# Kernel optimization log

Hardware: AMD Instinct MI355X
Metric: run time of the kernel (lower is better)

The kernel has to match this reference:

```python
import jax, jax.numpy as jnp
import numpy as np

NV = 8192   # number of nodes
NE = 8192   # number of edges
IN_V = 512
OUT_V = 512
IN_E = 512
A_COEF = 0.5  # self.a ; self.b = 1 - a


def setup_inputs() -> dict:
    key = jax.random.key(0)
    k = jax.random.split(key, 8)
    stdv = 1.0 / np.sqrt(OUT_V)
    return {
        "H_v": jax.random.normal(k[0], (NV, IN_V), dtype=jnp.float32),
        "H_e": jax.random.normal(k[1], (NE, IN_E), dtype=jnp.float32),
        "adj_e": jax.random.uniform(k[2], (NE, NE), dtype=jnp.float32),
        "adj_v": jax.random.uniform(k[3], (NV, NV), dtype=jnp.float32),
        "T": jax.random.uniform(k[4], (NV, NE), dtype=jnp.float32),
        "weight": jax.random.uniform(k[5], (IN_V, OUT_V), minval=-stdv, maxval=stdv, dtype=jnp.float32),
        "p": jax.random.normal(k[6], (1, IN_E), dtype=jnp.float32),
        "bias": jax.random.uniform(k[7], (OUT_V,), minval=-stdv, maxval=stdv, dtype=jnp.float32),
    }


def reference(H_v, H_e, adj_e, adj_v, T, weight, p, bias):
    # node_layer=True path of GraphConvolution.forward
    # gate: per-edge scalar from H_e @ p^T  -> [Ne]
    gate = (H_e @ p.T)[:, 0]
    # T @ diag(gate) @ T^T computed as broadcast column-scale (same math,
    # avoids materializing the Ne x Ne diagonal)
    multiplier1 = (T * gate[None, :]) @ T.T            # [Nv, Nv]
    eye = jnp.eye(multiplier1.shape[0], dtype=multiplier1.dtype)
    M1 = eye + (1.0 - eye) * multiplier1
    adjusted_A = M1 * adj_v
    H_v_weight = H_v @ weight                          # [Nv, out_v]
    output = adjusted_A @ H_v_weight
    output1 = adj_v @ H_v_weight
    output = output * A_COEF + output1 * (1.0 - A_COEF)
    ret = output + bias
    return (ret, H_e)
```

## Files before the change

kernel.cpp:

```cpp
#include <hip/hip_runtime.h>
#include <hip/hip_bf16.h>

typedef __attribute__((ext_vector_type(4))) float  f32x4;
typedef __attribute__((ext_vector_type(8))) short  s16x8;
typedef __attribute__((ext_vector_type(4))) short  s16x4;

#define NV 8192
#define NE 8192
#define DIM 512

__device__ inline short f2bf(float x) {
    unsigned u = __float_as_uint(x);
    u += 0x7fffu + ((u >> 16) & 1u);
    return (short)(u >> 16);
}
__device__ inline float bf2f(short s) {
    return __uint_as_float(((unsigned)(unsigned short)s) << 16);
}

__global__ void gate_kernel(const float* __restrict__ He, const float* __restrict__ p,
                            float* __restrict__ gate) {
    int row  = blockIdx.x * 4 + (threadIdx.x >> 6);
    int lane = threadIdx.x & 63;
    const float* r = He + (size_t)row * DIM + lane * 8;
    float4 a0 = *(const float4*)r;
    float4 a1 = *(const float4*)(r + 4);
    float4 p0 = *(const float4*)(p + lane * 8);
    float4 p1 = *(const float4*)(p + lane * 8 + 4);
    float s = a0.x*p0.x + a0.y*p0.y + a0.z*p0.z + a0.w*p0.w
            + a1.x*p1.x + a1.y*p1.y + a1.z*p1.z + a1.w*p1.w;
    #pragma unroll
    for (int off = 32; off; off >>= 1) s += __shfl_down(s, off);
    if (lane == 0) gate[row] = s;
}

__global__ void convert_T(const float* __restrict__ T, const float* __restrict__ gate,
                          short* __restrict__ Tg, short* __restrict__ Tb) {
    size_t gid  = (size_t)blockIdx.x * blockDim.x + threadIdx.x;
    size_t base = gid * 8;
    int col = (int)(base & (NE - 1));
    float4 t0 = *(const float4*)(T + base);
    float4 t1 = *(const float4*)(T + base + 4);
    float4 g0 = *(const float4*)(gate + col);
    float4 g1 = *(const float4*)(gate + col + 4);
    s16x8 vb, vg;
    vb[0]=f2bf(t0.x); vb[1]=f2bf(t0.y); vb[2]=f2bf(t0.z); vb[3]=f2bf(t0.w);
    vb[4]=f2bf(t1.x); vb[5]=f2bf(t1.y); vb[6]=f2bf(t1.z); vb[7]=f2bf(t1.w);
    vg[0]=f2bf(t0.x*g0.x); vg[1]=f2bf(t0.y*g0.y); vg[2]=f2bf(t0.z*g0.z); vg[3]=f2bf(t0.w*g0.w);
    vg[4]=f2bf(t1.x*g1.x); vg[5]=f2bf(t1.y*g1.y); vg[6]=f2bf(t1.z*g1.z); vg[7]=f2bf(t1.w*g1.w);
    *(s16x8*)(Tb + base) = vb;
    *(s16x8*)(Tg + base) = vg;
}

__global__ void to_bf16(const float* __restrict__ in, short* __restrict__ out) {
    size_t base = ((size_t)blockIdx.x * blockDim.x + threadIdx.x) * 8;
    float4 a = *(const float4*)(in + base);
    float4 b = *(const float4*)(in + base + 4);
    s16x8 v;
    v[0]=f2bf(a.x); v[1]=f2bf(a.y); v[2]=f2bf(a.z); v[3]=f2bf(a.w);
    v[4]=f2bf(b.x); v[5]=f2bf(b.y); v[6]=f2bf(b.z); v[7]=f2bf(b.w);
    *(s16x8*)(out + base) = v;
}

__global__ void wT_bf16(const float* __restrict__ W, short* __restrict__ WT) {
    __shared__ short t[64][65];
    int rb = blockIdx.x, cb = blockIdx.y;
    int c = threadIdx.x & 63, r0 = threadIdx.x >> 6;
    #pragma unroll
    for (int i = 0; i < 16; ++i) {
        int r = i * 4 + r0;
        t[r][c] = f2bf(W[(size_t)(rb * 64 + r) * DIM + cb * 64 + c]);
    }
    __syncthreads();
    #pragma unroll
    for (int i = 0; i < 16; ++i) {
        int r = i * 4 + r0;
        WT[(size_t)(cb * 64 + r) * DIM + rb * 64 + c] = t[c][r];
    }
}

template<int EPI>
__global__ __launch_bounds__(256)
void gemm_bt(const short* __restrict__ A, const short* __restrict__ B,
             int M, int N, int K,
             short* __restrict__ Cb,
             const float* __restrict__ bias, float* __restrict__ Cf) {
    __shared__ short As[128 * 32];
    __shared__ short Bs[128 * 32];

    int nwg = gridDim.x;
    int bid = blockIdx.x;
    int cpx = nwg >> 3;
    bid = (bid & 7) * cpx + (bid >> 3);

    const int nbn = N >> 7;
    const int bm = (bid / nbn) << 7;
    const int bn = (bid % nbn) << 7;
    const int tid  = threadIdx.x;
    const int lane = tid & 63;
    const int wave = tid >> 6;
    const int wrow = (wave >> 1) * 64;
    const int wcol = (wave & 1) * 64;

    f32x4 acc[4][4] = {};

    const int lrow = lane >> 2;
    const int lcol = ((lane & 3) ^ ((lrow >> 1) & 3)) * 8;

    for (int k0 = 0; k0 < K; k0 += 32) {
        #pragma unroll
        for (int it = 0; it < 2; ++it) {
            int chunk = it * 4 + wave;
            int row = chunk * 16 + lrow;
            __builtin_amdgcn_global_load_lds(
                (const __attribute__((address_space(1))) void*)(A + (size_t)(bm + row) * K + k0 + lcol),
                (__attribute__((address_space(3))) void*)(As + chunk * 512), 16, 0, 0);
            __builtin_amdgcn_global_load_lds(
                (const __attribute__((address_space(1))) void*)(B + (size_t)(bn + row) * K + k0 + lcol),
                (__attribute__((address_space(3))) void*)(Bs + chunk * 512), 16, 0, 0);
        }
        __syncthreads();

        const int fr = lane & 15;
        const int sw = (fr >> 1) & 3;
        const int sa = ((lane >> 4) ^ sw) * 8;
        s16x8 af[4], bfr[4];
        #pragma unroll
        for (int i = 0; i < 4; ++i) {
            af[i]  = *(const s16x8*)&As[(wrow + i * 16 + fr) * 32 + sa];
            bfr[i] = *(const s16x8*)&Bs[(wcol + i * 16 + fr) * 32 + sa];
        }
        #pragma unroll
        for (int i = 0; i < 4; ++i)
            #pragma unroll
            for (int j = 0; j < 4; ++j)
                acc[i][j] = __builtin_amdgcn_mfma_f32_16x16x32_bf16(af[i], bfr[j], acc[i][j], 0, 0, 0);
        __syncthreads();
    }

    const int fr = lane & 15, fq = (lane >> 4) * 4;
    #pragma unroll
    for (int i = 0; i < 4; ++i) {
        #pragma unroll
        for (int j = 0; j < 4; ++j) {
            int col = bn + wcol + j * 16 + fr;
            #pragma unroll
            for (int v = 0; v < 4; ++v) {
                int row = bm + wrow + i * 16 + fq + v;
                float d = acc[i][j][v];
                if (EPI == 1) Cf[(size_t)row * N + col] = d + bias[col];
                else          Cb[(size_t)row * N + col] = f2bf(d);
            }
        }
    }
}

#define FENCE asm volatile("" ::: "memory")
#define BAR   do { FENCE; __builtin_amdgcn_s_barrier(); FENCE; } while (0)
#define MFMA16(I0, J0)                                                                       \
    _Pragma("unroll") for (int x = 0; x < 4; ++x)                                            \
    _Pragma("unroll") for (int y = 0; y < 2; ++y)                                            \
    _Pragma("unroll") for (int s = 0; s < 2; ++s)                                            \
        acc[(I0)+x][(J0)+y] = __builtin_amdgcn_mfma_f32_16x16x32_bf16(                       \
            af[x][s], bf[(J0)+y][s], acc[(I0)+x][(J0)+y], 0, 0, 0);

#define GEMM256_CORE(NIT, KMASK)                                                             \
    stageA(0, 0, 0); stageA(0, 1, 0);                                                        \
    stageB(0, 0, 0); stageB(0, 1, 0);                                                        \
    stageB(1, 0, 1); stageB(1, 1, 1);                                                        \
    asm volatile("s_waitcnt vmcnt(4)" ::: "memory");                                         \
    __builtin_amdgcn_s_barrier();                                                            \
    FENCE;                                                                                   \
    _Pragma("unroll 1")                                                                      \
    for (int it = 0; it < (NIT); ++it) {                                                     \
        const int kt = it * 2;                                                               \
        _Pragma("unroll") for (int x = 0; x < 4; ++x) { af[x][0] = lda(A0o, x, 0); af[x][1] = lda(A0o, x, 1); } \
        _Pragma("unroll") for (int y = 0; y < 2; ++y) { bf[y][0] = ldb(B0o, y, 0); bf[y][1] = ldb(B0o, y, 1); } \
        stageA(1, 0, kt + 1);                                                                \
        asm volatile("s_waitcnt lgkmcnt(8)" ::: "memory");                                   \
        BAR; __builtin_amdgcn_s_setprio(1); MFMA16(0, 0) __builtin_amdgcn_s_setprio(0); BAR; \
        _Pragma("unroll") for (int y = 0; y < 2; ++y) { bf[2+y][0] = ldb(B0o, 2+y, 0); bf[2+y][1] = ldb(B0o, 2+y, 1); } \
        stageA(1, 1, kt + 1);                                                                \
        BAR; __builtin_amdgcn_s_setprio(1); MFMA16(0, 2) __builtin_amdgcn_s_setprio(0); BAR; \
        _Pragma("unroll") for (int x = 0; x < 4; ++x) { af[x][0] = lda(A0o, 4+x, 0); af[x][1] = lda(A0o, 4+x, 1); } \
        stageB(0, 0, kt + 2);                                                                \
        BAR; __builtin_amdgcn_s_setprio(1); MFMA16(4, 0) __builtin_amdgcn_s_setprio(0); BAR; \
        stageB(0, 1, kt + 2);                                                                \
        BAR; __builtin_amdgcn_s_setprio(1); MFMA16(4, 2) __builtin_amdgcn_s_setprio(0);      \
        asm volatile("s_waitcnt vmcnt(4)" ::: "memory"); BAR;                                \
        _Pragma("unroll") for (int x = 0; x < 4; ++x) { af[x][0] = lda(A1o, x, 0); af[x][1] = lda(A1o, x, 1); } \
        _Pragma("unroll") for (int y = 0; y < 2; ++y) { bf[y][0] = ldb(B1o, y, 0); bf[y][1] = ldb(B1o, y, 1); } \
        stageA(0, 0, kt + 2);                                                                \
        asm volatile("s_waitcnt lgkmcnt(8)" ::: "memory");                                   \
        BAR; __builtin_amdgcn_s_setprio(1); MFMA16(0, 0) __builtin_amdgcn_s_setprio(0); BAR; \
        _Pragma("unroll") for (int y = 0; y < 2; ++y) { bf[2+y][0] = ldb(B1o, 2+y, 0); bf[2+y][1] = ldb(B1o, 2+y, 1); } \
        stageA(0, 1, kt + 2);                                                                \
        BAR; __builtin_amdgcn_s_setprio(1); MFMA16(0, 2) __builtin_amdgcn_s_setprio(0); BAR; \
        _Pragma("unroll") for (int x = 0; x < 4; ++x) { af[x][0] = lda(A1o, 4+x, 0); af[x][1] = lda(A1o, 4+x, 1); } \
        stageB(1, 0, kt + 3);                                                                \
        BAR; __builtin_amdgcn_s_setprio(1); MFMA16(4, 0) __builtin_amdgcn_s_setprio(0); BAR; \
        stageB(1, 1, kt + 3);                                                                \
        BAR; __builtin_amdgcn_s_setprio(1); MFMA16(4, 2) __builtin_amdgcn_s_setprio(0);      \
        asm volatile("s_waitcnt vmcnt(4)" ::: "memory"); BAR;                                \
    }                                                                                        \
    asm volatile("s_waitcnt vmcnt(0)" ::: "memory");                                         \
    BAR;

#define GEMM256_PRELUDE(KMASK)                                                               \
    const int tid  = threadIdx.x;                                                            \
    const int wave = tid >> 6;                                                               \
    const int lane = tid & 63;                                                               \
    const int wm = wave >> 2;                                                                \
    const int wn = wave & 3;                                                                 \
    const int fr = lane & 15;                                                                \
    const int kq = lane >> 4;                                                                \
    const int lr = lane >> 3;                                                                \
    const int lsl = (lane & 7) ^ lr;                                                         \
    const int A0o = wm * 8192;                                                               \
    const int A1o = 16384 + wm * 8192;                                                       \
    const int B0o = 32768 + ((wn >> 1) << 13);                                               \
    const int B1o = B0o + 16384;                                                             \
    const short* aSrc = A + (size_t)(bm + wave * 8 + lr) * 8192 + kb + lsl * 8;              \
    const short* bSrc = B + (size_t)(bn + wave * 8 + lr) * 8192 + kb + lsl * 8;              \
    auto stageA = [&](int buf, int h, int kt) {                                              \
        const short* s0 = aSrc + ((size_t)h << 20) + ((kt << 6) & (KMASK));                  \
        short* d = &lds[buf * 16384 + h * 8192 + wave * 512];                                \
        __builtin_amdgcn_global_load_lds((const __attribute__((address_space(1))) void*)s0,  \
            (__attribute__((address_space(3))) void*)d, 16, 0, 0);                           \
        __builtin_amdgcn_global_load_lds((const __attribute__((address_space(1))) void*)(s0 + (size_t)(64 * 8192)), \
            (__attribute__((address_space(3))) void*)(d + 4096), 16, 0, 0);                  \
    };                                                                                       \
    auto stageB = [&](int buf, int h, int kt) {                                              \
        const short* s0 = bSrc + ((size_t)h << 20) + ((kt << 6) & (KMASK));                  \
        short* d = &lds[32768 + buf * 16384 + h * 8192 + wave * 512];                        \
        __builtin_amdgcn_global_load_lds((const __attribute__((address_space(1))) void*)s0,  \
            (__attribute__((address_space(3))) void*)d, 16, 0, 0);                           \
        __builtin_amdgcn_global_load_lds((const __attribute__((address_space(1))) void*)(s0 + (size_t)(64 * 8192)), \
            (__attribute__((address_space(3))) void*)(d + 4096), 16, 0, 0);                  \
    };                                                                                       \
    auto lda = [&](int base, int i, int ks) -> s16x8 {                                       \
        int rl = i * 16 + fr;                                                                \
        int slot = ((ks << 2) + kq) ^ (rl & 7);                                              \
        return *(const s16x8*)&lds[base + rl * 64 + slot * 8];                               \
    };                                                                                       \
    auto ldb = [&](int base, int j, int ks) -> s16x8 {                                       \
        int rl = ((wn & 1) << 6) + j * 16 + fr;                                              \
        int slot = ((ks << 2) + kq) ^ (rl & 7);                                              \
        return *(const s16x8*)&lds[base + rl * 64 + slot * 8];                               \
    };                                                                                       \
    f32x4 acc[8][4] = {};                                                                    \
    s16x8 af[4][2], bf[4][2];

__global__ __launch_bounds__(512, 2)
void gemm256(const short* __restrict__ A, const short* __restrict__ B,
             const float* __restrict__ adj, short* __restrict__ Cb) {
    __shared__ short lds[65536];

    int b = blockIdx.x;
    b = (b & 7) * 64 + (b >> 3);
    int bi, bj;
    if (b < 496) {
        int rem = b;
        bi = 0;
        while (rem >= 31 - bi) { rem -= 31 - bi; ++bi; }
        bj = bi + 1 + rem;
    } else {
        bi = bj = b - 496;
    }
    const int bm = bi << 8;
    const int bn = bj << 8;
    const int kb = 0;

    GEMM256_PRELUDE(8191)
    GEMM256_CORE(64, 8191)

    const int fq = kq << 2;
    #pragma unroll
    for (int i = 0; i < 8; ++i) {
        int rl0 = wm * 128 + i * 16 + fq;
        #pragma unroll
        for (int j = 0; j < 4; ++j) {
            int cl = wn * 64 + j * 16 + fr;
            #pragma unroll
            for (int v = 0; v < 4; ++v) {
                int rl = rl0 + v;
                lds[rl * 256 + (cl ^ ((rl & 7) << 3))] = f2bf(acc[i][j][v]);
            }
        }
    }
    BAR;

    const int rloc = tid >> 5;
    const int cc   = (tid & 31) * 8;
    #pragma unroll 4
    for (int m = 0; m < 16; ++m) {
        int r = m * 16 + rloc;
        s16x8 mv = *(const s16x8*)&lds[r * 256 + (cc ^ ((r & 7) << 3))];
        const float* arow = adj + (size_t)(bm + r) * 8192 + bn + cc;
        float4 a0 = *(const float4*)arow;
        float4 a1 = *(const float4*)(arow + 4);
        float av[8] = {a0.x,a0.y,a0.z,a0.w,a1.x,a1.y,a1.z,a1.w};
        s16x8 o;
        #pragma unroll
        for (int e = 0; e < 8; ++e) {
            float cv = av[e] * (0.5f * bf2f(mv[e]) + 0.5f);
            if (bm == bn && r == cc + e) cv = av[e];
            o[e] = f2bf(cv);
        }
        *(s16x8*)&Cb[(size_t)(bm + r) * 8192 + bn + cc] = o;
    }

    if (bm != bn) {
        #pragma unroll 1
        for (int h = 0; h < 2; ++h) {
            BAR;
            if ((wn >> 1) == h) {
                #pragma unroll
                for (int i = 0; i < 8; ++i) {
                    int r0 = wm * 128 + i * 16 + fq;
                    #pragma unroll
                    for (int j = 0; j < 4; ++j) {
                        int c = ((wn & 1) << 6) + j * 16 + fr;
                        s16x4 o4;
                        o4[0] = f2bf(acc[i][j][0]); o4[1] = f2bf(acc[i][j][1]);
                        o4[2] = f2bf(acc[i][j][2]); o4[3] = f2bf(acc[i][j][3]);
                        *(s16x4*)&lds[c * 264 + r0] = o4;
                    }
                }
            }
            BAR;
            const int r0 = (tid & 31) * 8;
            #pragma unroll 2
            for (int itr = 0; itr < 8; ++itr) {
                int c = itr * 16 + (tid >> 5);
                s16x8 mv = *(const s16x8*)&lds[c * 264 + r0];
                const float* arow = adj + (size_t)(bn + h * 128 + c) * 8192 + bm + r0;
                float4 a0 = *(const float4*)arow;
                float4 a1 = *(const float4*)(arow + 4);
                float av[8] = {a0.x,a0.y,a0.z,a0.w,a1.x,a1.y,a1.z,a1.w};
                s16x8 o;
                #pragma unroll
                for (int e = 0; e < 8; ++e)
                    o[e] = f2bf(av[e] * (0.5f * bf2f(mv[e]) + 0.5f));
                *(s16x8*)&Cb[(size_t)(bn + h * 128 + c) * 8192 + bm + r0] = o;
            }
        }
    }
}

__global__ __launch_bounds__(512, 2)
void gemm256_ks(const short* __restrict__ A, const short* __restrict__ B,
                float* __restrict__ part) {
    __shared__ short lds[65536];

    int b = blockIdx.x;
    const int t  = b >> 4;
    const int ks = b & 15;
    const int bm = (16 + t) << 8;
    const int bn = bm;
    const int kb = ks << 9;

    GEMM256_PRELUDE(511)
    GEMM256_CORE(4, 511)

    float* po = part + (size_t)(t * 16 + ks) * 65536;
    const int fq = kq << 2;
    #pragma unroll
    for (int i = 0; i < 8; ++i) {
        #pragma unroll
        for (int j = 0; j < 4; ++j) {
            int C = wn * 64 + j * 16 + fr;
            #pragma unroll
            for (int v = 0; v < 4; ++v) {
                int R = wm * 128 + i * 16 + fq + v;
                po[R * 256 + C] = acc[i][j][v];
            }
        }
    }
}

__global__ void reduce_diag(const float* __restrict__ part, const float* __restrict__ adj,
                            short* __restrict__ Cb) {
    int b = blockIdx.x;
    int t = b >> 5, sub = b & 31;
    int base = sub * 2048 + threadIdx.x * 8;
    int r = base >> 8, c = base & 255;
    const float* ps = part + (size_t)t * 16 * 65536 + base;
    float s[8] = {};
    #pragma unroll
    for (int ks = 0; ks < 16; ++ks) {
        f32x4 a = *(const f32x4*)(ps + (size_t)ks * 65536);
        f32x4 bq = *(const f32x4*)(ps + (size_t)ks * 65536 + 4);
        s[0]+=a[0]; s[1]+=a[1]; s[2]+=a[2]; s[3]+=a[3];
        s[4]+=bq[0]; s[5]+=bq[1]; s[6]+=bq[2]; s[7]+=bq[3];
    }
    int gr = (16 + t) * 256 + r, gc0 = (16 + t) * 256 + c;
    const float* arow = adj + (size_t)gr * 8192 + gc0;
    float4 a0 = *(const float4*)arow, a1 = *(const float4*)(arow + 4);
    float av[8] = {a0.x,a0.y,a0.z,a0.w,a1.x,a1.y,a1.z,a1.w};
    s16x8 o;
    #pragma unroll
    for (int e = 0; e < 8; ++e) {
        float cv = av[e] * (0.5f * s[e] + 0.5f);
        if (gr == gc0 + e) cv = av[e];
        o[e] = f2bf(cv);
    }
    *(s16x8*)&Cb[(size_t)gr * 8192 + gc0] = o;
}

__global__ __launch_bounds__(512, 2)
void gemm_fin(const short* __restrict__ A, const short* __restrict__ B,
              float* __restrict__ part) {
    __shared__ short lds[65536];

    int b = blockIdx.x;
    const int ks  = b & 3;
    const int bmi = (b >> 2) & 31;
    const int bni = b >> 7;
    const int bm = bmi << 8;
    const int bn = bni << 8;
    const int kb = ks << 11;

    GEMM256_PRELUDE(2047)
    GEMM256_CORE(16, 2047)

    float* po = part + ((size_t)(bmi * 2 + bni) * 4 + ks) * 65536;
    const int fq = kq << 2;
    #pragma unroll
    for (int i = 0; i < 8; ++i) {
        #pragma unroll
        for (int j = 0; j < 4; ++j) {
            int C = wn * 64 + j * 16 + fr;
            #pragma unroll
            for (int v = 0; v < 4; ++v) {
                int R = wm * 128 + i * 16 + fq + v;
                po[R * 256 + C] = acc[i][j][v];
            }
        }
    }
}

__global__ void reduce_out(const float* __restrict__ part, const float* __restrict__ bias,
                           float* __restrict__ out) {
    size_t g = ((size_t)blockIdx.x * 256 + threadIdx.x) * 8;
    int r = (int)(g >> 9);
    int c = (int)(g & 511);
    int tile = ((r >> 8) << 1) + (c >> 8);
    size_t inner = (size_t)(r & 255) * 256 + (c & 255);
    const float* ps = part + ((size_t)tile * 4) * 65536 + inner;
    float s[8] = {};
    #pragma unroll
    for (int ks = 0; ks < 4; ++ks) {
        f32x4 a = *(const f32x4*)(ps + (size_t)ks * 65536);
        f32x4 bq = *(const f32x4*)(ps + (size_t)ks * 65536 + 4);
        s[0]+=a[0]; s[1]+=a[1]; s[2]+=a[2]; s[3]+=a[3];
        s[4]+=bq[0]; s[5]+=bq[1]; s[6]+=bq[2]; s[7]+=bq[3];
    }
    float4 b0 = *(const float4*)(bias + c);
    float4 b1 = *(const float4*)(bias + c + 4);
    float bv[8] = {b0.x,b0.y,b0.z,b0.w,b1.x,b1.y,b1.z,b1.w};
    f32x4 o0, o1;
    o0[0]=s[0]+bv[0]; o0[1]=s[1]+bv[1]; o0[2]=s[2]+bv[2]; o0[3]=s[3]+bv[3];
    o1[0]=s[4]+bv[4]; o1[1]=s[5]+bv[5]; o1[2]=s[6]+bv[6]; o1[3]=s[7]+bv[7];
    *(f32x4*)(out + g) = o0;
    *(f32x4*)(out + g + 4) = o1;
}

extern "C" void kernel_launch(void* const* d_in, const int* in_sizes, int n_in,
                              void* d_out, int out_size, void* d_ws, size_t ws_size,
                              hipStream_t stream) {
    const float* Hv   = (const float*)d_in[0];
    const float* He   = (const float*)d_in[1];
    const float* adjv = (const float*)d_in[3];
    const float* T    = (const float*)d_in[4];
    const float* Wf   = (const float*)d_in[5];
    const float* p    = (const float*)d_in[6];
    const float* bias = (const float*)d_in[7];
    float* out = (float*)d_out;

    char* ws = (char*)d_ws;
    float* gate = (float*)(ws);
    short* Hvb  = (short*)(ws + 32768);
    short* Wt   = (short*)(ws + 8421376);
    short* Tg   = (short*)(ws + 16809984);
    short* Tb   = (short*)(ws + 151027712);
    short* Cb   = (short*)(ws + 285245440);
    short* WTb  = (short*)(ws + 285245440);
    float* part = (float*)(ws + 16809984);
    float* part2 = (float*)(ws + 16809984);

    hipMemcpyAsync(out + (size_t)NV * DIM, He, (size_t)NE * DIM * sizeof(float),
                   hipMemcpyDeviceToDevice, stream);

    gate_kernel<<<NE / 4, 256, 0, stream>>>(He, p, gate);
    convert_T<<<(NV * (NE / 8)) / 256, 256, 0, stream>>>(T, gate, Tg, Tb);
    to_bf16<<<(NV * DIM / 8) / 256, 256, 0, stream>>>(Hv, Hvb);
    wT_bf16<<<dim3(8, 8), 256, 0, stream>>>(Wf, WTb);

    gemm_bt<2><<<(DIM / 128) * (NV / 128), 256, 0, stream>>>(
        WTb, Hvb, DIM, NV, DIM, Wt, nullptr, nullptr);

    gemm256<<<512, 512, 0, stream>>>(Tg, Tb, adjv, Cb);
    gemm256_ks<<<256, 512, 0, stream>>>(Tg, Tb, part);
    reduce_diag<<<512, 256, 0, stream>>>(part, adjv, Cb);

    gemm_fin<<<256, 512, 0, stream>>>(Cb, Wt, part2);
    reduce_out<<<(NV * DIM / 8) / 256, 256, 0, stream>>>(part2, bias, out);
}
```

Baseline: 725.9 us.

## Triple-buffer A tiles in LDS with rotating slots for deeper prefetch

The A operand moves from a double-buffered to a triple-buffered LDS ring with three rotating slot bases (cA, cB, cC). Each A tile is now staged two k-steps ahead instead of one, and the vmcnt waits are relaxed from 4 to 8 so more global-to-LDS loads can stay in flight. B stays double-buffered and is moved to a higher LDS offset. LDS per block grows from 128KB to 160KB, which uses the full CU LDS and rules out a second resident block.

```diff
diff --git a/kernel.cpp b/kernel.cpp
--- a/kernel.cpp
+++ b/kernel.cpp
@@ -165,43 +165,46 @@
             af[x][s], bf[(J0)+y][s], acc[(I0)+x][(J0)+y], 0, 0, 0);
 
 #define GEMM256_CORE(NIT, KMASK)                                                             \
+    int cA = 0, cB = 16384, cC = 32768;                                                      \
     stageA(0, 0, 0); stageA(0, 1, 0);                                                        \
     stageB(0, 0, 0); stageB(0, 1, 0);                                                        \
+    stageA(16384, 0, 1); stageA(16384, 1, 1);                                                \
     stageB(1, 0, 1); stageB(1, 1, 1);                                                        \
-    asm volatile("s_waitcnt vmcnt(4)" ::: "memory");                                         \
+    asm volatile("s_waitcnt vmcnt(8)" ::: "memory");                                         \
     __builtin_amdgcn_s_barrier();                                                            \
     FENCE;                                                                                   \
     _Pragma("unroll 1")                                                                      \
     for (int it = 0; it < (NIT); ++it) {                                                     \
         const int kt = it * 2;                                                               \
-        _Pragma("unroll") for (int x = 0; x < 4; ++x) { af[x][0] = lda(A0o, x, 0); af[x][1] = lda(A0o, x, 1); } \
+        _Pragma("unroll") for (int x = 0; x < 4; ++x) { af[x][0] = lda(cA, x, 0); af[x][1] = lda(cA, x, 1); } \
         _Pragma("unroll") for (int y = 0; y < 2; ++y) { bf[y][0] = ldb(B0o, y, 0); bf[y][1] = ldb(B0o, y, 1); } \
-        stageA(1, 0, kt + 1);                                                                \
+        stageA(cC, 0, kt + 2);                                                               \
         asm volatile("s_waitcnt lgkmcnt(8)" ::: "memory");                                   \
         BAR; __builtin_amdgcn_s_setprio(1); MFMA16(0, 0) __builtin_amdgcn_s_setprio(0); BAR; \
         _Pragma("unroll") for (int y = 0; y < 2; ++y) { bf[2+y][0] = ldb(B0o, 2+y, 0); bf[2+y][1] = ldb(B0o, 2+y, 1); } \
-        stageA(1, 1, kt + 1);                                                                \
+        stageA(cC, 1, kt + 2);                                                               \
         BAR; __builtin_amdgcn_s_setprio(1); MFMA16(0, 2) __builtin_amdgcn_s_setprio(0); BAR; \
-        _Pragma("unroll") for (int x = 0; x < 4; ++x) { af[x][0] = lda(A0o, 4+x, 0); af[x][1] = lda(A0o, 4+x, 1); } \
+        _Pragma("unroll") for (int x = 0; x < 4; ++x) { af[x][0] = lda(cA, 4+x, 0); af[x][1] = lda(cA, 4+x, 1); } \
         stageB(0, 0, kt + 2);                                                                \
         BAR; __builtin_amdgcn_s_setprio(1); MFMA16(4, 0) __builtin_amdgcn_s_setprio(0); BAR; \
         stageB(0, 1, kt + 2);                                                                \
         BAR; __builtin_amdgcn_s_setprio(1); MFMA16(4, 2) __builtin_amdgcn_s_setprio(0);      \
-        asm volatile("s_waitcnt vmcnt(4)" ::: "memory"); BAR;                                \
-        _Pragma("unroll") for (int x = 0; x < 4; ++x) { af[x][0] = lda(A1o, x, 0); af[x][1] = lda(A1o, x, 1); } \
+        asm volatile("s_waitcnt vmcnt(8)" ::: "memory"); BAR;                                \
+        _Pragma("unroll") for (int x = 0; x < 4; ++x) { af[x][0] = lda(cB, x, 0); af[x][1] = lda(cB, x, 1); } \
         _Pragma("unroll") for (int y = 0; y < 2; ++y) { bf[y][0] = ldb(B1o, y, 0); bf[y][1] = ldb(B1o, y, 1); } \
-        stageA(0, 0, kt + 2);                                                                \
+        stageA(cA, 0, kt + 3);                                                               \
         asm volatile("s_waitcnt lgkmcnt(8)" ::: "memory");                                   \
         BAR; __builtin_amdgcn_s_setprio(1); MFMA16(0, 0) __builtin_amdgcn_s_setprio(0); BAR; \
         _Pragma("unroll") for (int y = 0; y < 2; ++y) { bf[2+y][0] = ldb(B1o, 2+y, 0); bf[2+y][1] = ldb(B1o, 2+y, 1); } \
-        stageA(0, 1, kt + 2);                                                                \
+        stageA(cA, 1, kt + 3);                                                               \
         BAR; __builtin_amdgcn_s_setprio(1); MFMA16(0, 2) __builtin_amdgcn_s_setprio(0); BAR; \
-        _Pragma("unroll") for (int x = 0; x < 4; ++x) { af[x][0] = lda(A1o, 4+x, 0); af[x][1] = lda(A1o, 4+x, 1); } \
+        _Pragma("unroll") for (int x = 0; x < 4; ++x) { af[x][0] = lda(cB, 4+x, 0); af[x][1] = lda(cB, 4+x, 1); } \
         stageB(1, 0, kt + 3);                                                                \
         BAR; __builtin_amdgcn_s_setprio(1); MFMA16(4, 0) __builtin_amdgcn_s_setprio(0); BAR; \
         stageB(1, 1, kt + 3);                                                                \
         BAR; __builtin_amdgcn_s_setprio(1); MFMA16(4, 2) __builtin_amdgcn_s_setprio(0);      \
-        asm volatile("s_waitcnt vmcnt(4)" ::: "memory"); BAR;                                \
+        asm volatile("s_waitcnt vmcnt(8)" ::: "memory"); BAR;                                \
+        int tRot = cA; cA = cC; cC = cB; cB = tRot;                                          \
     }                                                                                        \
     asm volatile("s_waitcnt vmcnt(0)" ::: "memory");                                         \
     BAR;
@@ -216,15 +219,14 @@
     const int kq = lane >> 4;                                                                \
     const int lr = lane >> 3;                                                                \
     const int lsl = (lane & 7) ^ lr;                                                         \
-    const int A0o = wm * 8192;                                                               \
-    const int A1o = 16384 + wm * 8192;                                                       \
-    const int B0o = 32768 + ((wn >> 1) << 13);                                               \
+    const int awm = wm * 8192;                                                               \
+    const int B0o = 49152 + ((wn >> 1) << 13);                                               \
     const int B1o = B0o + 16384;                                                             \
     const short* aSrc = A + (size_t)(bm + wave * 8 + lr) * 8192 + kb + lsl * 8;              \
     const short* bSrc = B + (size_t)(bn + wave * 8 + lr) * 8192 + kb + lsl * 8;              \
-    auto stageA = [&](int buf, int h, int kt) {                                              \
+    auto stageA = [&](int slotBase, int h, int kt) {                                         \
         const short* s0 = aSrc + ((size_t)h << 20) + ((kt << 6) & (KMASK));                  \
-        short* d = &lds[buf * 16384 + h * 8192 + wave * 512];                                \
+        short* d = &lds[slotBase + h * 8192 + wave * 512];                                   \
         __builtin_amdgcn_global_load_lds((const __attribute__((address_space(1))) void*)s0,  \
             (__attribute__((address_space(3))) void*)d, 16, 0, 0);                           \
         __builtin_amdgcn_global_load_lds((const __attribute__((address_space(1))) void*)(s0 + (size_t)(64 * 8192)), \
@@ -232,16 +234,16 @@
     };                                                                                       \
     auto stageB = [&](int buf, int h, int kt) {                                              \
         const short* s0 = bSrc + ((size_t)h << 20) + ((kt << 6) & (KMASK));                  \
-        short* d = &lds[32768 + buf * 16384 + h * 8192 + wave * 512];                        \
+        short* d = &lds[49152 + buf * 16384 + h * 8192 + wave * 512];                        \
         __builtin_amdgcn_global_load_lds((const __attribute__((address_space(1))) void*)s0,  \
             (__attribute__((address_space(3))) void*)d, 16, 0, 0);                           \
         __builtin_amdgcn_global_load_lds((const __attribute__((address_space(1))) void*)(s0 + (size_t)(64 * 8192)), \
             (__attribute__((address_space(3))) void*)(d + 4096), 16, 0, 0);                  \
     };                                                                                       \
-    auto lda = [&](int base, int i, int ks) -> s16x8 {                                       \
+    auto lda = [&](int cbase, int i, int ks) -> s16x8 {                                      \
         int rl = i * 16 + fr;                                                                \
         int slot = ((ks << 2) + kq) ^ (rl & 7);                                              \
-        return *(const s16x8*)&lds[base + rl * 64 + slot * 8];                               \
+        return *(const s16x8*)&lds[cbase + awm + rl * 64 + slot * 8];                        \
     };                                                                                       \
     auto ldb = [&](int base, int j, int ks) -> s16x8 {                                       \
         int rl = ((wn & 1) << 6) + j * 16 + fr;                                              \
@@ -254,7 +256,7 @@
 __global__ __launch_bounds__(512, 2)
 void gemm256(const short* __restrict__ A, const short* __restrict__ B,
              const float* __restrict__ adj, short* __restrict__ Cb) {
-    __shared__ short lds[65536];
+    __shared__ short lds[81920];
 
     int b = blockIdx.x;
     b = (b & 7) * 64 + (b >> 3);
@@ -351,7 +353,7 @@
 __global__ __launch_bounds__(512, 2)
 void gemm256_ks(const short* __restrict__ A, const short* __restrict__ B,
                 float* __restrict__ part) {
-    __shared__ short lds[65536];
+    __shared__ short lds[81920];
 
     int b = blockIdx.x;
     const int t  = b >> 4;
@@ -411,7 +413,7 @@
 __global__ __launch_bounds__(512, 2)
 void gemm_fin(const short* __restrict__ A, const short* __restrict__ B,
               float* __restrict__ part) {
-    __shared__ short lds[65536];
+    __shared__ short lds[81920];
 
     int b = blockIdx.x;
     const int ks  = b & 3;
```

Result: no change. 722.6 us (-0.5%).
